# Kernel optimization log

Measured on AMD Instinct MI355X. Metric: run time of the kernel, lower is better.

The kernel has to match this reference:

```python
import jax, jax.numpy as jnp
import numpy as np

B, N, DIM, HEADS = 2048, 64, 256, 8
WH = WW = 8  # window size; N = WH*WW


def _buffers():
    # continuous relative coords table [1, 2*WH-1, 2*WW-1, 2], log-scaled as in Swin-V2
    rh = np.arange(-(WH - 1), WH, dtype=np.float32)
    rw = np.arange(-(WW - 1), WW, dtype=np.float32)
    t = np.stack(np.meshgrid(rh, rw, indexing='ij'), axis=-1)[None]
    t[..., 0] /= (WH - 1)
    t[..., 1] /= (WW - 1)
    t *= 8.0
    t = np.sign(t) * np.log2(np.abs(t) + 1.0) / np.log2(8.0)
    # relative position index [N, N]
    ch, cw = np.arange(WH), np.arange(WW)
    coords = np.stack(np.meshgrid(ch, cw, indexing='ij')).reshape(2, -1)
    rel = (coords[:, :, None] - coords[:, None, :]).transpose(1, 2, 0)
    rel[..., 0] += WH - 1
    rel[..., 1] += WW - 1
    rel[..., 0] *= 2 * WW - 1
    idx = rel.sum(-1)
    return jnp.asarray(t, dtype=jnp.float32), jnp.asarray(idx, dtype=jnp.int32)


def setup_inputs() -> dict:
    key = jax.random.key(0)
    ks = jax.random.split(key, 8)
    tbl, idx = _buffers()
    return {
        'x': jax.random.normal(ks[0], (B, N, DIM), dtype=jnp.float32),
        'qkv_w': jax.random.normal(ks[1], (3 * DIM, DIM), dtype=jnp.float32) * 0.02,
        'q_bias': jnp.zeros((DIM,), dtype=jnp.float32),
        'v_bias': jnp.zeros((DIM,), dtype=jnp.float32),
        'scale': jnp.full((HEADS, 1, 1), np.log(10.0), dtype=jnp.float32),
        'cpb_w1': jax.random.normal(ks[2], (512, 2), dtype=jnp.float32) * 0.02,
        'cpb_b1': jnp.zeros((512,), dtype=jnp.float32),
        'cpb_w2': jax.random.normal(ks[3], (HEADS, 512), dtype=jnp.float32) * 0.02,
        'proj_w': jax.random.normal(ks[4], (DIM, DIM), dtype=jnp.float32) * 0.02,
        'proj_b': jnp.zeros((DIM,), dtype=jnp.float32),
        'rel_coords_table': tbl,
        'rel_pos_index': idx,
    }


def reference(x, qkv_w, q_bias, v_bias, scale, cpb_w1, cpb_b1, cpb_w2,
              proj_w, proj_b, rel_coords_table, rel_pos_index):
    b, n, c = x.shape
    h = scale.shape[0]
    d = c // h
    # qkv projection, bias = [q_bias, 0, v_bias]
    bias = jnp.concatenate([q_bias, jnp.zeros_like(v_bias), v_bias])
    qkv = x @ qkv_w.T + bias
    q, k, v = jnp.split(qkv, 3, axis=-1)
    to_heads = lambda t: t.reshape(b, n, h, d).transpose(0, 2, 1, 3)  # b h n d
    q, k, v = to_heads(q), to_heads(k), to_heads(v)
    # cosine attention: L2-normalize q, k (F.normalize eps=1e-12)
    l2n = lambda t: t / jnp.maximum(jnp.linalg.norm(t, axis=-1, keepdims=True), 1e-12)
    q, k = l2n(q), l2n(k)
    attn = jnp.einsum('bhnd,bhmd->bhnm', q, k)
    # clamped learnable log-temperature per head
    sc = jnp.exp(jnp.minimum(scale, jnp.log(jnp.float32(100.0))))  # [h,1,1]
    attn = attn * sc
    # continuous position bias: MLP(2->512->h), gathered by rel index, 16*sigmoid
    tbl = jax.nn.relu(rel_coords_table @ cpb_w1.T + cpb_b1) @ cpb_w2.T  # [1,15,15,h]
    tbl = tbl.reshape(-1, h)
    cpb = tbl[rel_pos_index.reshape(-1)].reshape(n, n, h).transpose(2, 0, 1)  # [h,n,n]
    attn = attn + 16.0 * jax.nn.sigmoid(cpb)[None]
    attn = jax.nn.softmax(attn, axis=-1)
    out = jnp.einsum('bhnm,bhmd->bhnd', attn, v)
    out = out.transpose(0, 2, 1, 3).reshape(b, n, c)
    return out @ proj_w.T + proj_b
```

## Files before the change

### kernel.cpp

```cpp
#include <hip/hip_runtime.h>
#include <stdint.h>

typedef unsigned short u16;
typedef unsigned int u32;
typedef short bf8_t __attribute__((ext_vector_type(8)));
typedef float f4_t  __attribute__((ext_vector_type(4)));
typedef float f16_t __attribute__((ext_vector_type(16)));

#define LOG2E 1.44269504088896340736f

static __device__ __forceinline__ u32 pkbf(float lo, float hi){
  u32 r; asm("v_cvt_pk_bf16_f32 %0, %1, %2" : "=v"(r) : "v"(lo), "v"(hi)); return r;
}

static __device__ __forceinline__ float pair_add(float v, bool hi5){
  union { float f; u32 u; } a; a.f = v;
  auto r = __builtin_amdgcn_permlane32_swap(a.u, a.u, false, false);
  union { u32 u; float f; } p; p.u = hi5 ? r[0] : r[1];
  return v + p.f;
}

static __device__ __forceinline__ void cvt_tile(const f16_t c, bf8_t& f0, bf8_t& f1){
  u32 p0 = pkbf(c[0], c[1]),  p1 = pkbf(c[2], c[3]);
  u32 p2 = pkbf(c[4], c[5]),  p3 = pkbf(c[6], c[7]);
  u32 p4 = pkbf(c[8], c[9]),  p5 = pkbf(c[10], c[11]);
  u32 p6 = pkbf(c[12], c[13]), p7 = pkbf(c[14], c[15]);
  auto r02 = __builtin_amdgcn_permlane32_swap(p0, p2, false, false);
  auto r13 = __builtin_amdgcn_permlane32_swap(p1, p3, false, false);
  auto r46 = __builtin_amdgcn_permlane32_swap(p4, p6, false, false);
  auto r57 = __builtin_amdgcn_permlane32_swap(p5, p7, false, false);
  union { u32 u[4]; bf8_t b; } x0, x1;
  x0.u[0] = r02[0]; x0.u[1] = r13[0]; x0.u[2] = r02[1]; x0.u[3] = r13[1];
  x1.u[0] = r46[0]; x1.u[1] = r57[0]; x1.u[2] = r46[1]; x1.u[3] = r57[1];
  f0 = x0.b; f1 = x1.b;
}

#define MFMA32(a, b, c) __builtin_amdgcn_mfma_f32_32x32x16_bf16(a, b, c, 0, 0, 0)


__global__ __launch_bounds__(256)
void prep_kernel(const float* __restrict__ qkvw, const float* __restrict__ projw,
                 const float* __restrict__ tab, const float* __restrict__ w1,
                 const float* __restrict__ b1, const float* __restrict__ w2,
                 u16* __restrict__ wpk, float* __restrict__ tbl){
  __shared__ float red[4][8];
  if (blockIdx.x < 128){
    int u = blockIdx.x * 256 + threadIdx.x;
    int hb  = u >> 10;
    int ks  = (u >> 6) & 15;
    int l5  = (u >> 5) & 1;
    int l31 = u & 31;
    int row = hb * 32 + l31, col = ks * 16 + l5 * 8;
    const float* src = (row < 768) ? (qkvw + (size_t)row * 256 + col)
                                   : (projw + (size_t)(row - 768) * 256 + col);
    float4 v0 = *reinterpret_cast<const float4*>(src);
    float4 v1 = *reinterpret_cast<const float4*>(src + 4);
    uint4 p;
    p.x = pkbf(v0.x, v0.y); p.y = pkbf(v0.z, v0.w);
    p.z = pkbf(v1.x, v1.y); p.w = pkbf(v1.z, v1.w);
    *reinterpret_cast<uint4*>(wpk + (size_t)u * 8) = p;
  } else {
    int i = blockIdx.x - 128;
    int tid = threadIdx.x;
    int wv = tid >> 6, lane = tid & 63;
    float c0 = tab[2*i], c1 = tab[2*i+1];
    int j0 = tid * 2;
    float4 w14 = *reinterpret_cast<const float4*>(w1 + 2*j0);
    float2 b12 = *reinterpret_cast<const float2*>(b1 + j0);
    float h0 = fmaxf(fmaf(c1, w14.y, fmaf(c0, w14.x, b12.x)), 0.f);
    float h1 = fmaxf(fmaf(c1, w14.w, fmaf(c0, w14.z, b12.y)), 0.f);
    float part[8];
    #pragma unroll
    for (int hh = 0; hh < 8; hh++){
      float2 w22 = *reinterpret_cast<const float2*>(w2 + hh*512 + j0);
      part[hh] = fmaf(h1, w22.y, h0 * w22.x);
    }
    #pragma unroll
    for (int hh = 0; hh < 8; hh++)
      #pragma unroll
      for (int off = 1; off < 64; off <<= 1)
        part[hh] += __shfl_xor(part[hh], off);
    if (lane == 0){
      #pragma unroll
      for (int hh = 0; hh < 8; hh++) red[wv][hh] = part[hh];
    }
    __syncthreads();
    if (tid < 8)
      tbl[i*8 + tid] = (red[0][tid] + red[1][tid]) + (red[2][tid] + red[3][tid]);
  }
}

__global__ void cpbgather_kernel(const float* __restrict__ tbl, const int* __restrict__ idx,
                                 const float* __restrict__ scale, float* __restrict__ biasF,
                                 float* __restrict__ scf){
  int u = blockIdx.x * blockDim.x + threadIdx.x;
  int rl   = u & 3;
  int lane = (u >> 2) & 63;
  int r4   = (u >> 8) & 3;
  int tile = (u >> 10) & 3;
  int hh   = (u >> 12) & 7;
  int qt = tile & 1, kt = tile >> 1;
  int query = 32*qt + (lane & 31);
  int key   = 32*kt + rl + 8*r4 + 4*(lane >> 5);
  int id = idx[query*64 + key];
  float xv = tbl[id*8 + hh];
  float s = 1.f / (1.f + expf(-xv));
  biasF[u] = 16.f * s * LOG2E;
  if (u < 8){
    float sc = fminf(scale[u], 4.6051701859880913680f);
    scf[u] = expf(sc) * LOG2E;
  }
}

#define XS 264

__global__ __launch_bounds__(512, 4)
void winattn_kernel(const float* __restrict__ x, const u16* __restrict__ wpk,
                    const float* __restrict__ qb, const float* __restrict__ vbias,
                    const float* __restrict__ biasF, const float* __restrict__ scf,
                    const float* __restrict__ projb, float* __restrict__ out){
  __shared__ u16 xlds[64 * XS];
  __shared__ u16 olds[64 * XS];

  const int b = blockIdx.x;
  const int t = threadIdx.x;
  const int w = t >> 6, lane = t & 63;
  const int l31 = lane & 31, l5 = lane >> 5;
  const bool hi5 = (l5 != 0);
  const int h = w;
  const int fragoff = l5 * 256 + l31 * 8;

  {
    const f4_t* xg = reinterpret_cast<const f4_t*>(x + (size_t)b * 16384);
    #pragma unroll
    for (int i = 0; i < 8; i++){
      int fi = t + 512 * i;
      f4_t v = __builtin_nontemporal_load(xg + fi);
      uint2 p; p.x = pkbf(v[0], v[1]); p.y = pkbf(v[2], v[3]);
      int row = fi >> 6, c = (fi & 63) * 4;
      *reinterpret_cast<uint2*>(&xlds[row * XS + c]) = p;
    }
  }
  __syncthreads();

  bf8_t qf00, qf01, qf10, qf11;
  bf8_t kf00, kf01, kf10, kf11;
  bf8_t vf0, vf1, vf2, vf3;
  const float qs = scf[h];

  {
    f16_t cq0, cq1, ck0, ck1;
    #pragma unroll
    for (int r = 0; r < 16; r++){
      float bqr = qb[32*h + (r & 3) + 8*(r >> 2) + 4*l5];
      cq0[r] = bqr; cq1[r] = bqr; ck0[r] = 0.f; ck1[r] = 0.f;
    }
    const u16* wqf = wpk + (size_t)h * 8192 + fragoff;
    const u16* wkf = wqf + (size_t)8 * 8192;
    #pragma unroll 4
    for (int ks = 0; ks < 16; ks++){
      const int ko = ks * 16 + 8 * l5;
      bf8_t aq  = *reinterpret_cast<const bf8_t*>(wqf + ks * 512);
      bf8_t ak  = *reinterpret_cast<const bf8_t*>(wkf + ks * 512);
      bf8_t bx0 = *reinterpret_cast<const bf8_t*>(&xlds[l31 * XS + ko]);
      bf8_t bx1 = *reinterpret_cast<const bf8_t*>(&xlds[(32 + l31) * XS + ko]);
      cq0 = MFMA32(aq, bx0, cq0);
      cq1 = MFMA32(aq, bx1, cq1);
      ck0 = MFMA32(ak, bx0, ck0);
      ck1 = MFMA32(ak, bx1, ck1);
    }
    {
      float sq = 0.f, sk = 0.f;
      #pragma unroll
      for (int r = 0; r < 16; r++){ sq = fmaf(cq0[r], cq0[r], sq); sk = fmaf(ck0[r], ck0[r], sk); }
      sq = pair_add(sq, hi5); sk = pair_add(sk, hi5);
      float iq = qs * __builtin_amdgcn_rsqf(fmaxf(sq, 1e-24f));
      float ik = __builtin_amdgcn_rsqf(fmaxf(sk, 1e-24f));
      #pragma unroll
      for (int r = 0; r < 16; r++){ cq0[r] *= iq; ck0[r] *= ik; }
      cvt_tile(cq0, qf00, qf01);
      cvt_tile(ck0, kf00, kf01);
    }
    {
      float sq = 0.f, sk = 0.f;
      #pragma unroll
      for (int r = 0; r < 16; r++){ sq = fmaf(cq1[r], cq1[r], sq); sk = fmaf(ck1[r], ck1[r], sk); }
      sq = pair_add(sq, hi5); sk = pair_add(sk, hi5);
      float iq = qs * __builtin_amdgcn_rsqf(fmaxf(sq, 1e-24f));
      float ik = __builtin_amdgcn_rsqf(fmaxf(sk, 1e-24f));
      #pragma unroll
      for (int r = 0; r < 16; r++){ cq1[r] *= iq; ck1[r] *= ik; }
      cvt_tile(cq1, qf10, qf11);
      cvt_tile(ck1, kf10, kf11);
    }
  }

  {
    f16_t cv0, cv1;
    float bv = vbias[32*h + l31];
    #pragma unroll
    for (int r = 0; r < 16; r++){ cv0[r] = bv; cv1[r] = bv; }
    const u16* wvf = wpk + (size_t)(16 + h) * 8192 + fragoff;
    #pragma unroll 4
    for (int ks = 0; ks < 16; ks++){
      const int ko = ks * 16 + 8 * l5;
      bf8_t bw  = *reinterpret_cast<const bf8_t*>(wvf + ks * 512);
      bf8_t ax0 = *reinterpret_cast<const bf8_t*>(&xlds[l31 * XS + ko]);
      bf8_t ax1 = *reinterpret_cast<const bf8_t*>(&xlds[(32 + l31) * XS + ko]);
      cv0 = MFMA32(ax0, bw, cv0);
      cv1 = MFMA32(ax1, bw, cv1);
    }
    cvt_tile(cv0, vf0, vf1);
    cvt_tile(cv1, vf2, vf3);
  }

  const float shift = qs + 24.0f;
  #pragma unroll
  for (int nt = 0; nt < 2; nt++){
    union { f16_t c; f4_t q[4]; } S0, S1;
    {
      const f4_t* bf0 = reinterpret_cast<const f4_t*>(biasF) + (h*4 + nt    ) * 256 + lane;
      const f4_t* bf1 = reinterpret_cast<const f4_t*>(biasF) + (h*4 + 2 + nt) * 256 + lane;
      #pragma unroll
      for (int r4 = 0; r4 < 4; r4++){ S0.q[r4] = bf0[r4 * 64]; S1.q[r4] = bf1[r4 * 64]; }
    }
    f16_t s0 = S0.c, s1 = S1.c;
    bf8_t qfa = nt ? qf10 : qf00, qfb = nt ? qf11 : qf01;
    s0 = MFMA32(kf00, qfa, s0); s0 = MFMA32(kf01, qfb, s0);
    s1 = MFMA32(kf10, qfa, s1); s1 = MFMA32(kf11, qfb, s1);
    #pragma unroll
    for (int r = 0; r < 16; r++){
      s0[r] = __builtin_amdgcn_exp2f(s0[r] - shift);
      s1[r] = __builtin_amdgcn_exp2f(s1[r] - shift);
    }
    float a0 = 0.f, a1 = 0.f, a2 = 0.f, a3 = 0.f;
    #pragma unroll
    for (int r4 = 0; r4 < 4; r4++){
      a0 += s0[4*r4 + 0] + s1[4*r4 + 0];
      a1 += s0[4*r4 + 1] + s1[4*r4 + 1];
      a2 += s0[4*r4 + 2] + s1[4*r4 + 2];
      a3 += s0[4*r4 + 3] + s1[4*r4 + 3];
    }
    float ssum = pair_add((a0 + a1) + (a2 + a3), hi5);
    float invr = __builtin_amdgcn_rcpf(ssum);
    bf8_t pf0, pf1, pf2, pf3;
    cvt_tile(s0, pf0, pf1);
    cvt_tile(s1, pf2, pf3);
    f16_t co;
    #pragma unroll
    for (int r = 0; r < 16; r++) co[r] = 0.f;
    co = MFMA32(vf0, pf0, co); co = MFMA32(vf1, pf1, co);
    co = MFMA32(vf2, pf2, co); co = MFMA32(vf3, pf3, co);
    #pragma unroll
    for (int r4 = 0; r4 < 4; r4++){
      uint2 p;
      p.x = pkbf(co[4*r4 + 0] * invr, co[4*r4 + 1] * invr);
      p.y = pkbf(co[4*r4 + 2] * invr, co[4*r4 + 3] * invr);
      *reinterpret_cast<uint2*>(&olds[(32*nt + l31) * XS + 32*h + 8*r4 + 4*l5]) = p;
    }
  }
  __syncthreads();

  {
    f16_t cp0, cp1;
    float pbv = projb[32*w + l31];
    #pragma unroll
    for (int r = 0; r < 16; r++){ cp0[r] = pbv; cp1[r] = pbv; }
    const u16* wpf = wpk + (size_t)(24 + w) * 8192 + fragoff;
    #pragma unroll 4
    for (int ks = 0; ks < 16; ks++){
      const int ko = ks * 16 + 8 * l5;
      bf8_t bw = *reinterpret_cast<const bf8_t*>(wpf + ks * 512);
      bf8_t a0 = *reinterpret_cast<const bf8_t*>(&olds[l31 * XS + ko]);
      bf8_t a1 = *reinterpret_cast<const bf8_t*>(&olds[(32 + l31) * XS + ko]);
      cp0 = MFMA32(a0, bw, cp0);
      cp1 = MFMA32(a1, bw, cp1);
    }
    float* og = out + (size_t)b * 16384;
    #pragma unroll
    for (int r = 0; r < 16; r++){
      int m = (r & 3) + 8*(r >> 2) + 4*l5;
      __builtin_nontemporal_store(cp0[r], &og[m * 256 + 32*w + l31]);
      __builtin_nontemporal_store(cp1[r], &og[(32 + m) * 256 + 32*w + l31]);
    }
  }
}

extern "C" void kernel_launch(void* const* d_in, const int* in_sizes, int n_in,
                              void* d_out, int out_size, void* d_ws, size_t ws_size,
                              hipStream_t stream){
  const float* x     = (const float*)d_in[0];
  const float* qkvw  = (const float*)d_in[1];
  const float* qb    = (const float*)d_in[2];
  const float* vb    = (const float*)d_in[3];
  const float* scale = (const float*)d_in[4];
  const float* w1    = (const float*)d_in[5];
  const float* b1    = (const float*)d_in[6];
  const float* w2    = (const float*)d_in[7];
  const float* pw    = (const float*)d_in[8];
  const float* pb    = (const float*)d_in[9];
  const float* tab   = (const float*)d_in[10];
  const int*   idx   = (const int*)d_in[11];
  float* out = (float*)d_out;

  char* ws = (char*)d_ws;
  u16*   wpkp = (u16*)ws;
  float* bias = (float*)(ws + 524288);
  float* tbl  = (float*)(ws + 655360);
  float* scfp = (float*)(ws + 662560);

  hipLaunchKernelGGL(prep_kernel,     dim3(353), dim3(256), 0, stream,
                     qkvw, pw, tab, w1, b1, w2, wpkp, tbl);
  hipLaunchKernelGGL(cpbgather_kernel,dim3(128), dim3(256), 0, stream, tbl, idx, scale, bias, scfp);
  hipLaunchKernelGGL(winattn_kernel,  dim3(2048), dim3(512), 0, stream,
                     x, wpkp, qb, vb, bias, scfp, pb, out);
}
```

Measured before the change: 115.1 us.

## Process two windows per block to reuse weight fragments and share LDS

Each block now handles two windows, so every Q, V and projection weight fragment loaded from global memory feeds MFMAs for both windows. The K projection is computed per window just before use to limit register pressure, and the attention output overwrites the x buffer in LDS instead of using a separate buffer. The grid is halved, which reduces block count and parallelism, and register pressure rises from holding Q and V fragments for two windows.

New measurement: 114.0 us. About the same (-0.9%).

```diff
diff --git a/kernel.cpp b/kernel.cpp
--- a/kernel.cpp
+++ b/kernel.cpp
@@ -119,10 +119,9 @@
                     const float* __restrict__ qb, const float* __restrict__ vbias,
                     const float* __restrict__ biasF, const float* __restrict__ scf,
                     const float* __restrict__ projb, float* __restrict__ out){
-  __shared__ u16 xlds[64 * XS];
-  __shared__ u16 olds[64 * XS];
-
-  const int b = blockIdx.x;
+  __shared__ u16 xlds[2][64 * XS];
+
+  const int b0 = blockIdx.x * 2;
   const int t = threadIdx.x;
   const int w = t >> 6, lane = t & 63;
   const int l31 = lane & 31, l5 = lane >> 5;
@@ -130,158 +129,191 @@
   const int h = w;
   const int fragoff = l5 * 256 + l31 * 8;
 
-  {
-    const f4_t* xg = reinterpret_cast<const f4_t*>(x + (size_t)b * 16384);
+  #pragma unroll
+  for (int ww = 0; ww < 2; ww++){
+    const f4_t* xg = reinterpret_cast<const f4_t*>(x + (size_t)(b0 + ww) * 16384);
     #pragma unroll
     for (int i = 0; i < 8; i++){
       int fi = t + 512 * i;
       f4_t v = __builtin_nontemporal_load(xg + fi);
       uint2 p; p.x = pkbf(v[0], v[1]); p.y = pkbf(v[2], v[3]);
-      int row = fi >> 6, c = (fi & 63) * 4;
-      *reinterpret_cast<uint2*>(&xlds[row * XS + c]) = p;
+      *reinterpret_cast<uint2*>(&xlds[ww][(fi >> 6) * XS + (fi & 63) * 4]) = p;
     }
   }
   __syncthreads();
 
-  bf8_t qf00, qf01, qf10, qf11;
-  bf8_t kf00, kf01, kf10, kf11;
-  bf8_t vf0, vf1, vf2, vf3;
+  bf8_t qf[2][4], vf[2][4];
   const float qs = scf[h];
+  const float shift = qs + 24.0f;
 
   {
-    f16_t cq0, cq1, ck0, ck1;
+    f16_t cq[2][2];
     #pragma unroll
     for (int r = 0; r < 16; r++){
       float bqr = qb[32*h + (r & 3) + 8*(r >> 2) + 4*l5];
-      cq0[r] = bqr; cq1[r] = bqr; ck0[r] = 0.f; ck1[r] = 0.f;
+      cq[0][0][r] = bqr; cq[0][1][r] = bqr; cq[1][0][r] = bqr; cq[1][1][r] = bqr;
     }
     const u16* wqf = wpk + (size_t)h * 8192 + fragoff;
-    const u16* wkf = wqf + (size_t)8 * 8192;
     #pragma unroll 4
     for (int ks = 0; ks < 16; ks++){
+      bf8_t aq = *reinterpret_cast<const bf8_t*>(wqf + ks * 512);
       const int ko = ks * 16 + 8 * l5;
-      bf8_t aq  = *reinterpret_cast<const bf8_t*>(wqf + ks * 512);
-      bf8_t ak  = *reinterpret_cast<const bf8_t*>(wkf + ks * 512);
-      bf8_t bx0 = *reinterpret_cast<const bf8_t*>(&xlds[l31 * XS + ko]);
-      bf8_t bx1 = *reinterpret_cast<const bf8_t*>(&xlds[(32 + l31) * XS + ko]);
-      cq0 = MFMA32(aq, bx0, cq0);
-      cq1 = MFMA32(aq, bx1, cq1);
-      ck0 = MFMA32(ak, bx0, ck0);
-      ck1 = MFMA32(ak, bx1, ck1);
-    }
-    {
-      float sq = 0.f, sk = 0.f;
-      #pragma unroll
-      for (int r = 0; r < 16; r++){ sq = fmaf(cq0[r], cq0[r], sq); sk = fmaf(ck0[r], ck0[r], sk); }
-      sq = pair_add(sq, hi5); sk = pair_add(sk, hi5);
-      float iq = qs * __builtin_amdgcn_rsqf(fmaxf(sq, 1e-24f));
-      float ik = __builtin_amdgcn_rsqf(fmaxf(sk, 1e-24f));
-      #pragma unroll
-      for (int r = 0; r < 16; r++){ cq0[r] *= iq; ck0[r] *= ik; }
-      cvt_tile(cq0, qf00, qf01);
-      cvt_tile(ck0, kf00, kf01);
-    }
-    {
-      float sq = 0.f, sk = 0.f;
-      #pragma unroll
-      for (int r = 0; r < 16; r++){ sq = fmaf(cq1[r], cq1[r], sq); sk = fmaf(ck1[r], ck1[r], sk); }
-      sq = pair_add(sq, hi5); sk = pair_add(sk, hi5);
-      float iq = qs * __builtin_amdgcn_rsqf(fmaxf(sq, 1e-24f));
-      float ik = __builtin_amdgcn_rsqf(fmaxf(sk, 1e-24f));
-      #pragma unroll
-      for (int r = 0; r < 16; r++){ cq1[r] *= iq; ck1[r] *= ik; }
-      cvt_tile(cq1, qf10, qf11);
-      cvt_tile(ck1, kf10, kf11);
-    }
+      #pragma unroll
+      for (int ww = 0; ww < 2; ww++){
+        bf8_t bx0 = *reinterpret_cast<const bf8_t*>(&xlds[ww][l31 * XS + ko]);
+        bf8_t bx1 = *reinterpret_cast<const bf8_t*>(&xlds[ww][(32 + l31) * XS + ko]);
+        cq[ww][0] = MFMA32(aq, bx0, cq[ww][0]);
+        cq[ww][1] = MFMA32(aq, bx1, cq[ww][1]);
+      }
+    }
+    #pragma unroll
+    for (int ww = 0; ww < 2; ww++)
+      #pragma unroll
+      for (int tt = 0; tt < 2; tt++){
+        float sq = 0.f;
+        #pragma unroll
+        for (int r = 0; r < 16; r++) sq = fmaf(cq[ww][tt][r], cq[ww][tt][r], sq);
+        sq = pair_add(sq, hi5);
+        float iq = qs * __builtin_amdgcn_rsqf(fmaxf(sq, 1e-24f));
+        #pragma unroll
+        for (int r = 0; r < 16; r++) cq[ww][tt][r] *= iq;
+        cvt_tile(cq[ww][tt], qf[ww][2*tt], qf[ww][2*tt + 1]);
+      }
   }
 
   {
-    f16_t cv0, cv1;
+    f16_t cv[2][2];
     float bv = vbias[32*h + l31];
     #pragma unroll
-    for (int r = 0; r < 16; r++){ cv0[r] = bv; cv1[r] = bv; }
+    for (int r = 0; r < 16; r++){
+      cv[0][0][r] = bv; cv[0][1][r] = bv; cv[1][0][r] = bv; cv[1][1][r] = bv;
+    }
     const u16* wvf = wpk + (size_t)(16 + h) * 8192 + fragoff;
     #pragma unroll 4
     for (int ks = 0; ks < 16; ks++){
+      bf8_t bw = *reinterpret_cast<const bf8_t*>(wvf + ks * 512);
       const int ko = ks * 16 + 8 * l5;
-      bf8_t bw  = *reinterpret_cast<const bf8_t*>(wvf + ks * 512);
-      bf8_t ax0 = *reinterpret_cast<const bf8_t*>(&xlds[l31 * XS + ko]);
-      bf8_t ax1 = *reinterpret_cast<const bf8_t*>(&xlds[(32 + l31) * XS + ko]);
-      cv0 = MFMA32(ax0, bw, cv0);
-      cv1 = MFMA32(ax1, bw, cv1);
-    }
-    cvt_tile(cv0, vf0, vf1);
-    cvt_tile(cv1, vf2, vf3);
-  }
-
-  const float shift = qs + 24.0f;
+      #pragma unroll
+      for (int ww = 0; ww < 2; ww++){
+        bf8_t ax0 = *reinterpret_cast<const bf8_t*>(&xlds[ww][l31 * XS + ko]);
+        bf8_t ax1 = *reinterpret_cast<const bf8_t*>(&xlds[ww][(32 + l31) * XS + ko]);
+        cv[ww][0] = MFMA32(ax0, bw, cv[ww][0]);
+        cv[ww][1] = MFMA32(ax1, bw, cv[ww][1]);
+      }
+    }
+    #pragma unroll
+    for (int ww = 0; ww < 2; ww++){
+      cvt_tile(cv[ww][0], vf[ww][0], vf[ww][1]);
+      cvt_tile(cv[ww][1], vf[ww][2], vf[ww][3]);
+    }
+  }
+
   #pragma unroll
-  for (int nt = 0; nt < 2; nt++){
-    union { f16_t c; f4_t q[4]; } S0, S1;
+  for (int ww = 0; ww < 2; ww++){
+    bf8_t kfw[4];
     {
-      const f4_t* bf0 = reinterpret_cast<const f4_t*>(biasF) + (h*4 + nt    ) * 256 + lane;
-      const f4_t* bf1 = reinterpret_cast<const f4_t*>(biasF) + (h*4 + 2 + nt) * 256 + lane;
-      #pragma unroll
-      for (int r4 = 0; r4 < 4; r4++){ S0.q[r4] = bf0[r4 * 64]; S1.q[r4] = bf1[r4 * 64]; }
-    }
-    f16_t s0 = S0.c, s1 = S1.c;
-    bf8_t qfa = nt ? qf10 : qf00, qfb = nt ? qf11 : qf01;
-    s0 = MFMA32(kf00, qfa, s0); s0 = MFMA32(kf01, qfb, s0);
-    s1 = MFMA32(kf10, qfa, s1); s1 = MFMA32(kf11, qfb, s1);
+      f16_t ck[2];
+      #pragma unroll
+      for (int r = 0; r < 16; r++){ ck[0][r] = 0.f; ck[1][r] = 0.f; }
+      const u16* wkf = wpk + (size_t)(8 + h) * 8192 + fragoff;
+      #pragma unroll 4
+      for (int ks = 0; ks < 16; ks++){
+        bf8_t ak = *reinterpret_cast<const bf8_t*>(wkf + ks * 512);
+        const int ko = ks * 16 + 8 * l5;
+        bf8_t bx0 = *reinterpret_cast<const bf8_t*>(&xlds[ww][l31 * XS + ko]);
+        bf8_t bx1 = *reinterpret_cast<const bf8_t*>(&xlds[ww][(32 + l31) * XS + ko]);
+        ck[0] = MFMA32(ak, bx0, ck[0]);
+        ck[1] = MFMA32(ak, bx1, ck[1]);
+      }
+      #pragma unroll
+      for (int tt = 0; tt < 2; tt++){
+        float sk = 0.f;
+        #pragma unroll
+        for (int r = 0; r < 16; r++) sk = fmaf(ck[tt][r], ck[tt][r], sk);
+        sk = pair_add(sk, hi5);
+        float ik = __builtin_amdgcn_rsqf(fmaxf(sk, 1e-24f));
+        #pragma unroll
+        for (int r = 0; r < 16; r++) ck[tt][r] *= ik;
+        cvt_tile(ck[tt], kfw[2*tt], kfw[2*tt + 1]);
+      }
+    }
+    __syncthreads();
+
+    #pragma unroll
+    for (int nt = 0; nt < 2; nt++){
+      union { f16_t c; f4_t q[4]; } S0, S1;
+      {
+        const f4_t* bf0 = reinterpret_cast<const f4_t*>(biasF) + (h*4 + nt    ) * 256 + lane;
+        const f4_t* bf1 = reinterpret_cast<const f4_t*>(biasF) + (h*4 + 2 + nt) * 256 + lane;
+        #pragma unroll
+        for (int r4 = 0; r4 < 4; r4++){ S0.q[r4] = bf0[r4 * 64]; S1.q[r4] = bf1[r4 * 64]; }
+      }
+      f16_t s0 = S0.c, s1 = S1.c;
+      s0 = MFMA32(kfw[0], qf[ww][2*nt], s0); s0 = MFMA32(kfw[1], qf[ww][2*nt+1], s0);
+      s1 = MFMA32(kfw[2], qf[ww][2*nt], s1); s1 = MFMA32(kfw[3], qf[ww][2*nt+1], s1);
+      #pragma unroll
+      for (int r = 0; r < 16; r++){
+        s0[r] = __builtin_amdgcn_exp2f(s0[r] - shift);
+        s1[r] = __builtin_amdgcn_exp2f(s1[r] - shift);
+      }
+      float a0 = 0.f, a1 = 0.f, a2 = 0.f, a3 = 0.f;
+      #pragma unroll
+      for (int r4 = 0; r4 < 4; r4++){
+        a0 += s0[4*r4 + 0] + s1[4*r4 + 0];
+        a1 += s0[4*r4 + 1] + s1[4*r4 + 1];
+        a2 += s0[4*r4 + 2] + s1[4*r4 + 2];
+        a3 += s0[4*r4 + 3] + s1[4*r4 + 3];
+      }
+      float ssum = pair_add((a0 + a1) + (a2 + a3), hi5);
+      float invr = __builtin_amdgcn_rcpf(ssum);
+      bf8_t pf0, pf1, pf2, pf3;
+      cvt_tile(s0, pf0, pf1);
+      cvt_tile(s1, pf2, pf3);
+      f16_t co;
+      #pragma unroll
+      for (int r = 0; r < 16; r++) co[r] = 0.f;
+      co = MFMA32(vf[ww][0], pf0, co); co = MFMA32(vf[ww][1], pf1, co);
+      co = MFMA32(vf[ww][2], pf2, co); co = MFMA32(vf[ww][3], pf3, co);
+      #pragma unroll
+      for (int r4 = 0; r4 < 4; r4++){
+        uint2 p;
+        p.x = pkbf(co[4*r4 + 0] * invr, co[4*r4 + 1] * invr);
+        p.y = pkbf(co[4*r4 + 2] * invr, co[4*r4 + 3] * invr);
+        *reinterpret_cast<uint2*>(&xlds[ww][(32*nt + l31) * XS + 32*h + 8*r4 + 4*l5]) = p;
+      }
+    }
+  }
+  __syncthreads();
+
+  {
+    f16_t cp[2][2];
+    float pbv = projb[32*w + l31];
     #pragma unroll
     for (int r = 0; r < 16; r++){
-      s0[r] = __builtin_amdgcn_exp2f(s0[r] - shift);
-      s1[r] = __builtin_amdgcn_exp2f(s1[r] - shift);
-    }
-    float a0 = 0.f, a1 = 0.f, a2 = 0.f, a3 = 0.f;
-    #pragma unroll
-    for (int r4 = 0; r4 < 4; r4++){
-      a0 += s0[4*r4 + 0] + s1[4*r4 + 0];
-      a1 += s0[4*r4 + 1] + s1[4*r4 + 1];
-      a2 += s0[4*r4 + 2] + s1[4*r4 + 2];
-      a3 += s0[4*r4 + 3] + s1[4*r4 + 3];
-    }
-    float ssum = pair_add((a0 + a1) + (a2 + a3), hi5);
-    float invr = __builtin_amdgcn_rcpf(ssum);
-    bf8_t pf0, pf1, pf2, pf3;
-    cvt_tile(s0, pf0, pf1);
-    cvt_tile(s1, pf2, pf3);
-    f16_t co;
-    #pragma unroll
-    for (int r = 0; r < 16; r++) co[r] = 0.f;
-    co = MFMA32(vf0, pf0, co); co = MFMA32(vf1, pf1, co);
-    co = MFMA32(vf2, pf2, co); co = MFMA32(vf3, pf3, co);
-    #pragma unroll
-    for (int r4 = 0; r4 < 4; r4++){
-      uint2 p;
-      p.x = pkbf(co[4*r4 + 0] * invr, co[4*r4 + 1] * invr);
-      p.y = pkbf(co[4*r4 + 2] * invr, co[4*r4 + 3] * invr);
-      *reinterpret_cast<uint2*>(&olds[(32*nt + l31) * XS + 32*h + 8*r4 + 4*l5]) = p;
-    }
-  }
-  __syncthreads();
-
-  {
-    f16_t cp0, cp1;
-    float pbv = projb[32*w + l31];
-    #pragma unroll
-    for (int r = 0; r < 16; r++){ cp0[r] = pbv; cp1[r] = pbv; }
+      cp[0][0][r] = pbv; cp[0][1][r] = pbv; cp[1][0][r] = pbv; cp[1][1][r] = pbv;
+    }
     const u16* wpf = wpk + (size_t)(24 + w) * 8192 + fragoff;
     #pragma unroll 4
     for (int ks = 0; ks < 16; ks++){
+      bf8_t bw = *reinterpret_cast<const bf8_t*>(wpf + ks * 512);
       const int ko = ks * 16 + 8 * l5;
-      bf8_t bw = *reinterpret_cast<const bf8_t*>(wpf + ks * 512);
-      bf8_t a0 = *reinterpret_cast<const bf8_t*>(&olds[l31 * XS + ko]);
-      bf8_t a1 = *reinterpret_cast<const bf8_t*>(&olds[(32 + l31) * XS + ko]);
-      cp0 = MFMA32(a0, bw, cp0);
-      cp1 = MFMA32(a1, bw, cp1);
-    }
-    float* og = out + (size_t)b * 16384;
-    #pragma unroll
-    for (int r = 0; r < 16; r++){
-      int m = (r & 3) + 8*(r >> 2) + 4*l5;
-      __builtin_nontemporal_store(cp0[r], &og[m * 256 + 32*w + l31]);
-      __builtin_nontemporal_store(cp1[r], &og[(32 + m) * 256 + 32*w + l31]);
+      #pragma unroll
+      for (int ww = 0; ww < 2; ww++){
+        bf8_t a0 = *reinterpret_cast<const bf8_t*>(&xlds[ww][l31 * XS + ko]);
+        bf8_t a1 = *reinterpret_cast<const bf8_t*>(&xlds[ww][(32 + l31) * XS + ko]);
+        cp[ww][0] = MFMA32(a0, bw, cp[ww][0]);
+        cp[ww][1] = MFMA32(a1, bw, cp[ww][1]);
+      }
+    }
+    #pragma unroll
+    for (int ww = 0; ww < 2; ww++){
+      float* og = out + (size_t)(b0 + ww) * 16384;
+      #pragma unroll
+      for (int r = 0; r < 16; r++){
+        int m = (r & 3) + 8*(r >> 2) + 4*l5;
+        __builtin_nontemporal_store(cp[ww][0][r], &og[m * 256 + 32*w + l31]);
+        __builtin_nontemporal_store(cp[ww][1][r], &og[(32 + m) * 256 + 32*w + l31]);
+      }
     }
   }
 }
@@ -312,6 +344,6 @@
   hipLaunchKernelGGL(prep_kernel,     dim3(353), dim3(256), 0, stream,
                      qkvw, pw, tab, w1, b1, w2, wpkp, tbl);
   hipLaunchKernelGGL(cpbgather_kernel,dim3(128), dim3(256), 0, stream, tbl, idx, scale, bias, scfp);
-  hipLaunchKernelGGL(winattn_kernel,  dim3(2048), dim3(512), 0, stream,
+  hipLaunchKernelGGL(winattn_kernel,  dim3(1024), dim3(512), 0, stream,
                      x, wpkp, qb, vb, bias, scfp, pb, out);
 }
```

## Split Q and K projections, add MFMA setprio, fold softmax shift into bias

Applied to the files above, without the earlier changes.

The fused Q/K projection loop becomes two sequential loops, so only two accumulator tiles are live at a time instead of four, which lowers register pressure at launch bound 512x4. s_setprio is raised around each MFMA loop so waves issuing matrix ops get priority over other waves. The constant softmax shift (scale plus 24) is now subtracted once in the precomputed bias table, removing one subtraction per score element. The cost is a second pass over the x tile in LDS for the K projection.

New measurement: 115.5 us. No clear change (+0.4%).

```diff
diff --git a/kernel.cpp b/kernel.cpp
--- a/kernel.cpp
+++ b/kernel.cpp
@@ -105,11 +105,9 @@
   int id = idx[query*64 + key];
   float xv = tbl[id*8 + hh];
   float s = 1.f / (1.f + expf(-xv));
-  biasF[u] = 16.f * s * LOG2E;
-  if (u < 8){
-    float sc = fminf(scale[u], 4.6051701859880913680f);
-    scf[u] = expf(sc) * LOG2E;
-  }
+  float qsh = expf(fminf(scale[hh], 4.6051701859880913680f)) * LOG2E;
+  biasF[u] = 16.f * s * LOG2E - (qsh + 24.0f);
+  if (u < 8) scf[u] = qsh;
 }
 
 #define XS 264
@@ -137,61 +135,92 @@
       int fi = t + 512 * i;
       f4_t v = __builtin_nontemporal_load(xg + fi);
       uint2 p; p.x = pkbf(v[0], v[1]); p.y = pkbf(v[2], v[3]);
-      int row = fi >> 6, c = (fi & 63) * 4;
-      *reinterpret_cast<uint2*>(&xlds[row * XS + c]) = p;
+      *reinterpret_cast<uint2*>(&xlds[(fi >> 6) * XS + (fi & 63) * 4]) = p;
     }
   }
   __syncthreads();
 
-  bf8_t qf00, qf01, qf10, qf11;
-  bf8_t kf00, kf01, kf10, kf11;
+  bf8_t qf0, qf1, qf2, qf3;
+  bf8_t kf0, kf1, kf2, kf3;
   bf8_t vf0, vf1, vf2, vf3;
   const float qs = scf[h];
 
   {
-    f16_t cq0, cq1, ck0, ck1;
+    f16_t cq0, cq1;
     #pragma unroll
     for (int r = 0; r < 16; r++){
       float bqr = qb[32*h + (r & 3) + 8*(r >> 2) + 4*l5];
-      cq0[r] = bqr; cq1[r] = bqr; ck0[r] = 0.f; ck1[r] = 0.f;
+      cq0[r] = bqr; cq1[r] = bqr;
     }
     const u16* wqf = wpk + (size_t)h * 8192 + fragoff;
-    const u16* wkf = wqf + (size_t)8 * 8192;
+    __builtin_amdgcn_s_setprio(1);
     #pragma unroll 4
     for (int ks = 0; ks < 16; ks++){
       const int ko = ks * 16 + 8 * l5;
       bf8_t aq  = *reinterpret_cast<const bf8_t*>(wqf + ks * 512);
-      bf8_t ak  = *reinterpret_cast<const bf8_t*>(wkf + ks * 512);
       bf8_t bx0 = *reinterpret_cast<const bf8_t*>(&xlds[l31 * XS + ko]);
       bf8_t bx1 = *reinterpret_cast<const bf8_t*>(&xlds[(32 + l31) * XS + ko]);
       cq0 = MFMA32(aq, bx0, cq0);
       cq1 = MFMA32(aq, bx1, cq1);
+    }
+    __builtin_amdgcn_s_setprio(0);
+    {
+      float sq = 0.f;
+      #pragma unroll
+      for (int r = 0; r < 16; r++) sq = fmaf(cq0[r], cq0[r], sq);
+      sq = pair_add(sq, hi5);
+      float iq = qs * __builtin_amdgcn_rsqf(fmaxf(sq, 1e-24f));
+      #pragma unroll
+      for (int r = 0; r < 16; r++) cq0[r] *= iq;
+      cvt_tile(cq0, qf0, qf1);
+    }
+    {
+      float sq = 0.f;
+      #pragma unroll
+      for (int r = 0; r < 16; r++) sq = fmaf(cq1[r], cq1[r], sq);
+      sq = pair_add(sq, hi5);
+      float iq = qs * __builtin_amdgcn_rsqf(fmaxf(sq, 1e-24f));
+      #pragma unroll
+      for (int r = 0; r < 16; r++) cq1[r] *= iq;
+      cvt_tile(cq1, qf2, qf3);
+    }
+  }
+
+  {
+    f16_t ck0, ck1;
+    #pragma unroll
+    for (int r = 0; r < 16; r++){ ck0[r] = 0.f; ck1[r] = 0.f; }
+    const u16* wkf = wpk + (size_t)(8 + h) * 8192 + fragoff;
+    __builtin_amdgcn_s_setprio(1);
+    #pragma unroll 4
+    for (int ks = 0; ks < 16; ks++){
+      const int ko = ks * 16 + 8 * l5;
+      bf8_t ak  = *reinterpret_cast<const bf8_t*>(wkf + ks * 512);
+      bf8_t bx0 = *reinterpret_cast<const bf8_t*>(&xlds[l31 * XS + ko]);
+      bf8_t bx1 = *reinterpret_cast<const bf8_t*>(&xlds[(32 + l31) * XS + ko]);
       ck0 = MFMA32(ak, bx0, ck0);
       ck1 = MFMA32(ak, bx1, ck1);
     }
-    {
-      float sq = 0.f, sk = 0.f;
-      #pragma unroll
-      for (int r = 0; r < 16; r++){ sq = fmaf(cq0[r], cq0[r], sq); sk = fmaf(ck0[r], ck0[r], sk); }
-      sq = pair_add(sq, hi5); sk = pair_add(sk, hi5);
-      float iq = qs * __builtin_amdgcn_rsqf(fmaxf(sq, 1e-24f));
+    __builtin_amdgcn_s_setprio(0);
+    {
+      float sk = 0.f;
+      #pragma unroll
+      for (int r = 0; r < 16; r++) sk = fmaf(ck0[r], ck0[r], sk);
+      sk = pair_add(sk, hi5);
       float ik = __builtin_amdgcn_rsqf(fmaxf(sk, 1e-24f));
       #pragma unroll
-      for (int r = 0; r < 16; r++){ cq0[r] *= iq; ck0[r] *= ik; }
-      cvt_tile(cq0, qf00, qf01);
-      cvt_tile(ck0, kf00, kf01);
-    }
-    {
-      float sq = 0.f, sk = 0.f;
-      #pragma unroll
-      for (int r = 0; r < 16; r++){ sq = fmaf(cq1[r], cq1[r], sq); sk = fmaf(ck1[r], ck1[r], sk); }
-      sq = pair_add(sq, hi5); sk = pair_add(sk, hi5);
-      float iq = qs * __builtin_amdgcn_rsqf(fmaxf(sq, 1e-24f));
+      for (int r = 0; r < 16; r++) ck0[r] *= ik;
+      cvt_tile(ck0, kf0, kf1);
+    }
+    {
+      float sk = 0.f;
+      #pragma unroll
+      for (int r = 0; r < 16; r++) sk = fmaf(ck1[r], ck1[r], sk);
+      sk = pair_add(sk, hi5);
       float ik = __builtin_amdgcn_rsqf(fmaxf(sk, 1e-24f));
       #pragma unroll
-      for (int r = 0; r < 16; r++){ cq1[r] *= iq; ck1[r] *= ik; }
-      cvt_tile(cq1, qf10, qf11);
-      cvt_tile(ck1, kf10, kf11);
+      for (int r = 0; r < 16; r++) ck1[r] *= ik;
+      cvt_tile(ck1, kf2, kf3);
     }
   }
 
@@ -201,6 +230,7 @@
     #pragma unroll
     for (int r = 0; r < 16; r++){ cv0[r] = bv; cv1[r] = bv; }
     const u16* wvf = wpk + (size_t)(16 + h) * 8192 + fragoff;
+    __builtin_amdgcn_s_setprio(1);
     #pragma unroll 4
     for (int ks = 0; ks < 16; ks++){
       const int ko = ks * 16 + 8 * l5;
@@ -210,11 +240,11 @@
       cv0 = MFMA32(ax0, bw, cv0);
       cv1 = MFMA32(ax1, bw, cv1);
     }
+    __builtin_amdgcn_s_setprio(0);
     cvt_tile(cv0, vf0, vf1);
     cvt_tile(cv1, vf2, vf3);
   }
 
-  const float shift = qs + 24.0f;
   #pragma unroll
   for (int nt = 0; nt < 2; nt++){
     union { f16_t c; f4_t q[4]; } S0, S1;
@@ -225,13 +255,15 @@
       for (int r4 = 0; r4 < 4; r4++){ S0.q[r4] = bf0[r4 * 64]; S1.q[r4] = bf1[r4 * 64]; }
     }
     f16_t s0 = S0.c, s1 = S1.c;
-    bf8_t qfa = nt ? qf10 : qf00, qfb = nt ? qf11 : qf01;
-    s0 = MFMA32(kf00, qfa, s0); s0 = MFMA32(kf01, qfb, s0);
-    s1 = MFMA32(kf10, qfa, s1); s1 = MFMA32(kf11, qfb, s1);
+    bf8_t qfa = nt ? qf2 : qf0, qfb = nt ? qf3 : qf1;
+    __builtin_amdgcn_s_setprio(1);
+    s0 = MFMA32(kf0, qfa, s0); s0 = MFMA32(kf1, qfb, s0);
+    s1 = MFMA32(kf2, qfa, s1); s1 = MFMA32(kf3, qfb, s1);
+    __builtin_amdgcn_s_setprio(0);
     #pragma unroll
     for (int r = 0; r < 16; r++){
-      s0[r] = __builtin_amdgcn_exp2f(s0[r] - shift);
-      s1[r] = __builtin_amdgcn_exp2f(s1[r] - shift);
+      s0[r] = __builtin_amdgcn_exp2f(s0[r]);
+      s1[r] = __builtin_amdgcn_exp2f(s1[r]);
     }
     float a0 = 0.f, a1 = 0.f, a2 = 0.f, a3 = 0.f;
     #pragma unroll
@@ -249,8 +281,10 @@
     f16_t co;
     #pragma unroll
     for (int r = 0; r < 16; r++) co[r] = 0.f;
+    __builtin_amdgcn_s_setprio(1);
     co = MFMA32(vf0, pf0, co); co = MFMA32(vf1, pf1, co);
     co = MFMA32(vf2, pf2, co); co = MFMA32(vf3, pf3, co);
+    __builtin_amdgcn_s_setprio(0);
     #pragma unroll
     for (int r4 = 0; r4 < 4; r4++){
       uint2 p;
@@ -267,6 +301,7 @@
     #pragma unroll
     for (int r = 0; r < 16; r++){ cp0[r] = pbv; cp1[r] = pbv; }
     const u16* wpf = wpk + (size_t)(24 + w) * 8192 + fragoff;
+    __builtin_amdgcn_s_setprio(1);
     #pragma unroll 4
     for (int ks = 0; ks < 16; ks++){
       const int ko = ks * 16 + 8 * l5;
@@ -276,6 +311,7 @@
       cp0 = MFMA32(a0, bw, cp0);
       cp1 = MFMA32(a1, bw, cp1);
     }
+    __builtin_amdgcn_s_setprio(0);
     float* og = out + (size_t)b * 16384;
     #pragma unroll
     for (int r = 0; r < 16; r++){
```
